# Kernel optimization log

Hardware: AMD Instinct MI355X
Metric: run time of the kernel (lower is better)

The kernel has to match this reference:

```python
import jax, jax.numpy as jnp
import numpy as np

C = 128      # block channels
K = 7        # involution kernel size
GC = 16      # group_ch
G = (C // 2) // GC  # involution groups = 4


def conv1x1(x, w, b):
    # x: (B,Cin,H,W), w: (Cout,Cin)
    return jnp.einsum('bchw,oc->bohw', x, w) + b[None, :, None, None]


def conv2d(x, w, b, pad):
    y = jax.lax.conv_general_dilated(
        x, w, window_strides=(1, 1), padding=((pad, pad), (pad, pad)),
        dimension_numbers=('NCHW', 'OIHW', 'NCHW'))
    return y + b[None, :, None, None]


def prelu(x, a):
    return jnp.where(x >= 0, x, a * x)


def patches7(x):
    # x: (B,C,H,W) -> (B,C,K*K,H,W), same padding (torch Unfold, pad=3)
    B, Cc, H, W = x.shape
    p = K // 2
    xp = jnp.pad(x, ((0, 0), (0, 0), (p, p), (p, p)))
    return jnp.stack([xp[:, :, i:i + H, j:j + W]
                      for i in range(K) for j in range(K)], axis=2)


def setup_inputs() -> dict:
    key = jax.random.key(0)
    ks = jax.random.split(key, 9)
    f32 = jnp.float32
    def w(k, shape, s=0.02):
        return jax.random.normal(k, shape, f32) * s
    d = {}
    d['x'] = jax.random.normal(ks[0], (2, C, 128, 128), f32)
    # conv1: C -> C//2, 1x1
    d['w1'] = w(ks[1], (C // 2, C)); d['b1'] = jnp.zeros((C // 2,), f32)
    d['a1'] = jnp.float32(0.25)  # PReLU (single param)
    # involution reduce: C//2 -> C//4, 1x1 (+ReLU)
    d['wr'] = w(ks[2], (C // 4, C // 2)); d['br'] = jnp.zeros((C // 4,), f32)
    # involution span: C//4 -> G*K*K, 1x1
    d['ws'] = w(ks[3], (G * K * K, C // 4)); d['bs'] = jnp.zeros((G * K * K,), f32)
    d['a2'] = jnp.float32(0.25)
    # conv2: C//2 -> C, 1x1
    d['w2'] = w(ks[4], (C, C // 2)); d['b2'] = jnp.zeros((C,), f32)
    # attn conv: 2 -> 1, 7x7 pad 3
    d['wa'] = w(ks[5], (1, 2, 7, 7)); d['ba'] = jnp.zeros((1,), f32)
    # psec: 3x3 (C//4->C//4) + PReLU + 1x1 (C//4->C)
    d['wp1'] = w(ks[6], (C // 4, C // 4, 3, 3)); d['bp1'] = jnp.zeros((C // 4,), f32)
    d['ap'] = jnp.float32(0.25)
    d['wp2'] = w(ks[7], (C, C // 4)); d['bp2'] = jnp.zeros((C,), f32)
    return d


def reference(x, w1, b1, a1, wr, br, ws, bs, a2, w2, b2, wa, ba, wp1, bp1, ap, wp2, bp2):
    B, _, H, W = x.shape
    x1 = prelu(conv1x1(x, w1, b1), a1)                       # (B, C/2, H, W)
    # involution: per-pixel dynamic kernels
    f = jax.nn.relu(conv1x1(x1, wr, br))                     # (B, C/4, H, W)
    kw = conv1x1(f, ws, bs).reshape(B, G, 1, K * K, H, W)    # dynamic kernels
    pat = patches7(x1).reshape(B, G, GC, K * K, H, W)        # unfolded patches
    x2 = (kw * pat).sum(axis=3).reshape(B, C // 2, H, W)     # multiply-reduce
    x3 = conv1x1(prelu(x2, a2), w2, b2)                      # (B, C, H, W)
    # attention gate on f (ZPool -> 7x7 conv -> sigmoid)
    zp = jnp.concatenate([f.max(axis=1, keepdims=True),
                          f.mean(axis=1, keepdims=True)], axis=1)
    attn = jax.nn.sigmoid(conv2d(zp, wa, ba, 3))             # (B, 1, H, W)
    x4 = x3 * attn
    ps = conv1x1(prelu(conv2d(f, wp1, bp1, 1), ap), wp2, bp2)
    return x4 + ps
```

## Files before the change

kernel.cpp:

```cpp
#include <hip/hip_runtime.h>

#define HW_  16384
#define NPX  32768

__device__ __forceinline__ float prelu_(float x, float a) { return x >= 0.f ? x : a * x; }

__global__ __launch_bounds__(256, 2) void k_conv1(const float* __restrict__ x,
        const float* __restrict__ w1, const float* __restrict__ b1,
        const float* __restrict__ a1p, float* __restrict__ x1) {
    __shared__ float xs[64 * 128];
    __shared__ float wT[128 * 36];
    int split = blockIdx.x >> 8;
    int tile = blockIdx.x & 255;
    int b = tile >> 7;
    int hw0 = (tile & 127) << 7;
    int o0 = split * 32;

    for (int e = threadIdx.x; e < 4096; e += 256) {
        int o = e >> 7, c = e & 127;
        wT[c * 36 + o] = w1[(o0 + o) * 128 + c];
    }
    int pxq = threadIdx.x & 31, outq = threadIdx.x >> 5;
    const float a1 = a1p[0];
    float4 acc[4];
    #pragma unroll
    for (int u = 0; u < 4; ++u) { float bv = b1[o0 + outq * 4 + u]; acc[u] = make_float4(bv, bv, bv, bv); }
    const float4* xb = (const float4*)(x + (b << 21) + hw0);
    #pragma unroll 1
    for (int half = 0; half < 2; ++half) {
        float4 xv[8];
        #pragma unroll
        for (int i = 0; i < 8; ++i) {
            int e = threadIdx.x + i * 256;
            int ch = e >> 5, pq = e & 31;
            xv[i] = xb[((half * 64 + ch) << 12) + pq];
        }
        #pragma unroll
        for (int i = 0; i < 8; ++i) {
            int e = threadIdx.x + i * 256;
            int ch = e >> 5, pq = e & 31;
            *(float4*)&xs[ch * 128 + pq * 4] = xv[i];
        }
        __syncthreads();
        #pragma unroll 8
        for (int c2 = 0; c2 < 64; ++c2) {
            float4 tap = *(const float4*)&xs[c2 * 128 + pxq * 4];
            float4 wv  = *(const float4*)&wT[(half * 64 + c2) * 36 + outq * 4];
            acc[0].x = fmaf(wv.x, tap.x, acc[0].x); acc[0].y = fmaf(wv.x, tap.y, acc[0].y);
            acc[0].z = fmaf(wv.x, tap.z, acc[0].z); acc[0].w = fmaf(wv.x, tap.w, acc[0].w);
            acc[1].x = fmaf(wv.y, tap.x, acc[1].x); acc[1].y = fmaf(wv.y, tap.y, acc[1].y);
            acc[1].z = fmaf(wv.y, tap.z, acc[1].z); acc[1].w = fmaf(wv.y, tap.w, acc[1].w);
            acc[2].x = fmaf(wv.z, tap.x, acc[2].x); acc[2].y = fmaf(wv.z, tap.y, acc[2].y);
            acc[2].z = fmaf(wv.z, tap.z, acc[2].z); acc[2].w = fmaf(wv.z, tap.w, acc[2].w);
            acc[3].x = fmaf(wv.w, tap.x, acc[3].x); acc[3].y = fmaf(wv.w, tap.y, acc[3].y);
            acc[3].z = fmaf(wv.w, tap.z, acc[3].z); acc[3].w = fmaf(wv.w, tap.w, acc[3].w);
        }
        __syncthreads();
    }
    #pragma unroll
    for (int u = 0; u < 4; ++u) {
        float4 r;
        r.x = prelu_(acc[u].x, a1); r.y = prelu_(acc[u].y, a1);
        r.z = prelu_(acc[u].z, a1); r.w = prelu_(acc[u].w, a1);
        *(float4*)(x1 + ((b * 64 + o0 + outq * 4 + u) << 14) + hw0 + pxq * 4) = r;
    }
}

__global__ __launch_bounds__(256, 4) void k_reduce(const float* __restrict__ x1,
        const float* __restrict__ wr, const float* __restrict__ br,
        float* __restrict__ f) {
    int tid = blockIdx.x * 256 + threadIdx.x;
    int p2 = tid & 16383;
    int q = tid >> 14;
    int b = p2 >> 13;
    int hw = (p2 & 8191) << 1;
    int o0 = q * 4;
    float2 acc[4];
    #pragma unroll
    for (int u = 0; u < 4; ++u) { float bv = br[o0 + u]; acc[u] = make_float2(bv, bv); }
    const float2* xp = (const float2*)(x1 + (b << 20) + hw);
    #pragma unroll 1
    for (int cb = 0; cb < 4; ++cb) {
        float2 xv[16];
        #pragma unroll
        for (int j = 0; j < 16; ++j) xv[j] = xp[(cb * 16 + j) << 13];
        #pragma unroll
        for (int j = 0; j < 16; ++j) {
            int c = cb * 16 + j;
            #pragma unroll
            for (int u = 0; u < 4; ++u) {
                float wv = wr[(o0 + u) * 64 + c];
                acc[u].x = fmaf(wv, xv[j].x, acc[u].x);
                acc[u].y = fmaf(wv, xv[j].y, acc[u].y);
            }
        }
    }
    float2* op = (float2*)(f + (b << 19) + hw);
    #pragma unroll
    for (int u = 0; u < 4; ++u) {
        float2 r;
        r.x = fmaxf(acc[u].x, 0.f); r.y = fmaxf(acc[u].y, 0.f);
        op[(o0 + u) << 13] = r;
    }
}

__global__ __launch_bounds__(256) void k_invol(const float* __restrict__ x1,
        const float* __restrict__ f, const float* __restrict__ ws_,
        const float* __restrict__ bs, float* __restrict__ x2,
        float* __restrict__ zp) {
    __shared__ float tile[16 * 22 * 24];
    int g = blockIdx.x >> 7;
    int t = blockIdx.x & 127;
    int b = t >> 6;
    int th = (t >> 3) & 7, tw = t & 7;
    int h0 = th * 16, w0 = tw * 16;
    const float* x1g = x1 + ((b * 64 + g * 16) << 14);
    #pragma unroll 1
    for (int rem = threadIdx.x; rem < 484; rem += 256) {
        int r = rem / 22, cl = rem - r * 22;
        int hh = h0 + r - 3, ww = w0 + cl - 3;
        bool ok = (hh >= 0 && hh < 128 && ww >= 0 && ww < 128);
        const float* src = x1g + (hh << 7) + ww;
        float v[16];
        #pragma unroll
        for (int c = 0; c < 16; ++c) v[c] = ok ? src[c << 14] : 0.f;
        float* dst = tile + r * 24 + cl;
        #pragma unroll
        for (int c = 0; c < 16; ++c) dst[c * 528] = v[c];
    }
    int lh = threadIdx.x >> 4, lw = threadIdx.x & 15;
    int hw = ((h0 + lh) << 7) + w0 + lw;
    float fv[32];
    const float* fp = f + (b << 19) + hw;
    #pragma unroll
    for (int c = 0; c < 32; ++c) fv[c] = fp[c << 14];
    if (g == 0) {
        float mx = fv[0], sm = fv[0];
        #pragma unroll
        for (int c = 1; c < 32; ++c) { mx = fmaxf(mx, fv[c]); sm += fv[c]; }
        zp[((b * 2 + 0) << 14) + hw] = mx;
        zp[((b * 2 + 1) << 14) + hw] = sm * (1.f / 32.f);
    }
    __syncthreads();
    float acc[16];
    #pragma unroll
    for (int u = 0; u < 16; ++u) acc[u] = 0.f;
    const float* tap0 = tile + lh * 24 + lw;
    const float* wk = ws_ + g * 49 * 32;
    const float* bsg = bs + g * 49;
    #pragma unroll 1
    for (int di = 0; di < 7; ++di) {
        #pragma unroll 1
        for (int dj = 0; dj < 7; ++dj) {
            int kk = di * 7 + dj;
            float kwv = bsg[kk];
            const float* wkk = wk + kk * 32;
            #pragma unroll
            for (int c = 0; c < 32; ++c) kwv = fmaf(wkk[c], fv[c], kwv);
            const float* tp = tap0 + di * 24 + dj;
            #pragma unroll
            for (int u = 0; u < 16; ++u)
                acc[u] = fmaf(kwv, tp[u * 528], acc[u]);
        }
    }
    float* op = x2 + ((b * 64 + g * 16) << 14) + hw;
    #pragma unroll
    for (int u = 0; u < 16; ++u) op[u << 14] = acc[u];
}

__global__ __launch_bounds__(256) void k_attn(const float* __restrict__ zp,
        const float* __restrict__ wa, const float* __restrict__ ba,
        float* __restrict__ attn) {
    __shared__ float zs[2][22 * 23];
    int t = blockIdx.x;
    int b = t >> 6;
    int tile = t & 63;
    int th = tile >> 3, tw = tile & 7;
    int h0 = th * 16, w0 = tw * 16;
    const float* zb = zp + (b << 15);
    #pragma unroll 1
    for (int rem = threadIdx.x; rem < 484; rem += 256) {
        int r = rem / 22, cl = rem - r * 22;
        int hh = h0 + r - 3, ww = w0 + cl - 3;
        bool ok = (hh >= 0 && hh < 128 && ww >= 0 && ww < 128);
        const float* src = zb + (hh << 7) + ww;
        float v0 = ok ? src[0] : 0.f;
        float v1 = ok ? src[HW_] : 0.f;
        zs[0][r * 23 + cl] = v0;
        zs[1][r * 23 + cl] = v1;
    }
    __syncthreads();
    int lh = threadIdx.x >> 4, lw = threadIdx.x & 15;
    float acc = ba[0];
    #pragma unroll
    for (int c = 0; c < 2; ++c) {
        const float* zc = &zs[c][lh * 23 + lw];
        #pragma unroll
        for (int i = 0; i < 7; ++i)
            #pragma unroll
            for (int j = 0; j < 7; ++j)
                acc = fmaf(wa[c * 49 + i * 7 + j], zc[i * 23 + j], acc);
    }
    attn[(b << 14) + ((h0 + lh) << 7) + w0 + lw] = 1.f / (1.f + expf(-acc));
}

__global__ __launch_bounds__(256) void k_psec1(const float* __restrict__ f,
        const float* __restrict__ wp1, const float* __restrict__ bp1,
        const float* __restrict__ app, float* __restrict__ p1) {
    __shared__ float fs[32 * 190];
    __shared__ float wT[288 * 16];
    int half = blockIdx.x >> 8;
    int t = blockIdx.x & 255;
    int b = t >> 7;
    int tile = t & 127;
    int th = tile >> 3, tw = tile & 7;
    int h0 = th * 8, w0 = tw * 16;
    int o0 = half * 16;

    const float4* wsrc4 = (const float4*)(wp1 + o0 * 288);
    #pragma unroll 1
    for (int e4 = threadIdx.x; e4 < 1152; e4 += 256) {
        float4 v = wsrc4[e4];
        int o = e4 / 72, r4 = (e4 - o * 72) * 4;
        wT[(r4 + 0) * 16 + o] = v.x;
        wT[(r4 + 1) * 16 + o] = v.y;
        wT[(r4 + 2) * 16 + o] = v.z;
        wT[(r4 + 3) * 16 + o] = v.w;
    }
    const float* fb = f + (b << 19);
    #pragma unroll 1
    for (int rem = threadIdx.x; rem < 180; rem += 256) {
        int r = rem / 18, cl = rem - r * 18;
        int hh = h0 + r - 1, ww = w0 + cl - 1;
        bool ok = (hh >= 0 && hh < 128 && ww >= 0 && ww < 128);
        const float* src = fb + (hh << 7) + ww;
        float* dst = fs + r * 19 + cl;
        #pragma unroll 1
        for (int cb = 0; cb < 4; ++cb) {
            float v[8];
            #pragma unroll
            for (int c = 0; c < 8; ++c) v[c] = ok ? src[(cb * 8 + c) << 14] : 0.f;
            #pragma unroll
            for (int c = 0; c < 8; ++c) dst[(cb * 8 + c) * 190] = v[c];
        }
    }
    __syncthreads();

    int pxq = threadIdx.x & 31;
    int rowq = pxq >> 2, colq = pxq & 3;
    int oh = threadIdx.x >> 5;
    const float ap = app[0];
    float acc[2][4];
    #pragma unroll
    for (int o = 0; o < 2; ++o) {
        float bv = bp1[o0 + oh * 2 + o];
        #pragma unroll
        for (int px = 0; px < 4; ++px) acc[o][px] = bv;
    }
    const float* fsb = fs + rowq * 19 + colq * 4;
    for (int ci = 0; ci < 32; ++ci) {
        float tap[3][6];
        const float* base = fsb + ci * 190;
        #pragma unroll
        for (int r = 0; r < 3; ++r)
            #pragma unroll
            for (int j = 0; j < 6; ++j)
                tap[r][j] = base[r * 19 + j];
        #pragma unroll
        for (int ki = 0; ki < 3; ++ki)
            #pragma unroll
            for (int kj = 0; kj < 3; ++kj) {
                float2 wv = *(const float2*)&wT[((ci * 9 + ki * 3 + kj) << 4) + oh * 2];
                #pragma unroll
                for (int px = 0; px < 4; ++px) {
                    float tv = tap[ki][px + kj];
                    acc[0][px] = fmaf(wv.x, tv, acc[0][px]);
                    acc[1][px] = fmaf(wv.y, tv, acc[1][px]);
                }
            }
    }
    int hw = ((h0 + rowq) << 7) + w0 + colq * 4;
    #pragma unroll
    for (int o = 0; o < 2; ++o) {
        float4 r;
        r.x = prelu_(acc[o][0], ap); r.y = prelu_(acc[o][1], ap);
        r.z = prelu_(acc[o][2], ap); r.w = prelu_(acc[o][3], ap);
        *(float4*)(p1 + ((b * 32 + o0 + oh * 2 + o) << 14) + hw) = r;
    }
}

__global__ __launch_bounds__(256, 2) void k_final(const float* __restrict__ x2,
        const float* __restrict__ p1, const float* __restrict__ attn,
        const float* __restrict__ a2p, const float* __restrict__ w2,
        const float* __restrict__ b2, const float* __restrict__ wp2,
        const float* __restrict__ bp2, float* __restrict__ out) {
    __shared__ float xs2[64 * 128];
    __shared__ float ps[32 * 128];
    __shared__ float wT2[64 * 36];
    __shared__ float wTp[32 * 36];
    __shared__ float as_[128];
    int split = blockIdx.x >> 8;
    int tile = blockIdx.x & 255;
    int b = tile >> 7;
    int hw0 = (tile & 127) << 7;
    int o0 = split * 32;
    const float a2 = a2p[0];

    for (int e = threadIdx.x; e < 2048; e += 256) {
        int o = e >> 6, c = e & 63;
        wT2[c * 36 + o] = w2[(o0 + o) * 64 + c];
    }
    for (int e = threadIdx.x; e < 1024; e += 256) {
        int o = e >> 5, c = e & 31;
        wTp[c * 36 + o] = wp2[(o0 + o) * 32 + c];
    }
    {
        const float4* xb = (const float4*)(x2 + (b << 20) + hw0);
        float4 xv[8];
        #pragma unroll
        for (int i = 0; i < 8; ++i) {
            int e = threadIdx.x + i * 256;
            xv[i] = xb[((e >> 5) << 12) + (e & 31)];
        }
        #pragma unroll
        for (int i = 0; i < 8; ++i) {
            int e = threadIdx.x + i * 256;
            float4 v = xv[i];
            v.x = prelu_(v.x, a2); v.y = prelu_(v.y, a2);
            v.z = prelu_(v.z, a2); v.w = prelu_(v.w, a2);
            *(float4*)&xs2[(e >> 5) * 128 + (e & 31) * 4] = v;
        }
        const float4* pb = (const float4*)(p1 + (b << 19) + hw0);
        float4 pv[4];
        #pragma unroll
        for (int i = 0; i < 4; ++i) {
            int e = threadIdx.x + i * 256;
            pv[i] = pb[((e >> 5) << 12) + (e & 31)];
        }
        #pragma unroll
        for (int i = 0; i < 4; ++i) {
            int e = threadIdx.x + i * 256;
            *(float4*)&ps[(e >> 5) * 128 + (e & 31) * 4] = pv[i];
        }
        if (threadIdx.x < 32)
            ((float4*)as_)[threadIdx.x] = ((const float4*)(attn + (b << 14) + hw0))[threadIdx.x];
    }
    int pxq = threadIdx.x & 31, outq = threadIdx.x >> 5;
    float b2v[4], bpv[4];
    #pragma unroll
    for (int u = 0; u < 4; ++u) { b2v[u] = b2[o0 + outq * 4 + u]; bpv[u] = bp2[o0 + outq * 4 + u]; }
    __syncthreads();

    float4 acc[4];
    #pragma unroll
    for (int u = 0; u < 4; ++u) acc[u] = make_float4(0.f, 0.f, 0.f, 0.f);
    #pragma unroll 8
    for (int c = 0; c < 64; ++c) {
        float4 tap = *(const float4*)&xs2[c * 128 + pxq * 4];
        float4 wv  = *(const float4*)&wT2[c * 36 + outq * 4];
        acc[0].x = fmaf(wv.x, tap.x, acc[0].x); acc[0].y = fmaf(wv.x, tap.y, acc[0].y);
        acc[0].z = fmaf(wv.x, tap.z, acc[0].z); acc[0].w = fmaf(wv.x, tap.w, acc[0].w);
        acc[1].x = fmaf(wv.y, tap.x, acc[1].x); acc[1].y = fmaf(wv.y, tap.y, acc[1].y);
        acc[1].z = fmaf(wv.y, tap.z, acc[1].z); acc[1].w = fmaf(wv.y, tap.w, acc[1].w);
        acc[2].x = fmaf(wv.z, tap.x, acc[2].x); acc[2].y = fmaf(wv.z, tap.y, acc[2].y);
        acc[2].z = fmaf(wv.z, tap.z, acc[2].z); acc[2].w = fmaf(wv.z, tap.w, acc[2].w);
        acc[3].x = fmaf(wv.w, tap.x, acc[3].x); acc[3].y = fmaf(wv.w, tap.y, acc[3].y);
        acc[3].z = fmaf(wv.w, tap.z, acc[3].z); acc[3].w = fmaf(wv.w, tap.w, acc[3].w);
    }
    float4 at = *(const float4*)&as_[pxq * 4];
    #pragma unroll
    for (int u = 0; u < 4; ++u) {
        acc[u].x = (acc[u].x + b2v[u]) * at.x + bpv[u];
        acc[u].y = (acc[u].y + b2v[u]) * at.y + bpv[u];
        acc[u].z = (acc[u].z + b2v[u]) * at.z + bpv[u];
        acc[u].w = (acc[u].w + b2v[u]) * at.w + bpv[u];
    }
    #pragma unroll 8
    for (int c = 0; c < 32; ++c) {
        float4 tap = *(const float4*)&ps[c * 128 + pxq * 4];
        float4 wv  = *(const float4*)&wTp[c * 36 + outq * 4];
        acc[0].x = fmaf(wv.x, tap.x, acc[0].x); acc[0].y = fmaf(wv.x, tap.y, acc[0].y);
        acc[0].z = fmaf(wv.x, tap.z, acc[0].z); acc[0].w = fmaf(wv.x, tap.w, acc[0].w);
        acc[1].x = fmaf(wv.y, tap.x, acc[1].x); acc[1].y = fmaf(wv.y, tap.y, acc[1].y);
        acc[1].z = fmaf(wv.y, tap.z, acc[1].z); acc[1].w = fmaf(wv.y, tap.w, acc[1].w);
        acc[2].x = fmaf(wv.z, tap.x, acc[2].x); acc[2].y = fmaf(wv.z, tap.y, acc[2].y);
        acc[2].z = fmaf(wv.z, tap.z, acc[2].z); acc[2].w = fmaf(wv.z, tap.w, acc[2].w);
        acc[3].x = fmaf(wv.w, tap.x, acc[3].x); acc[3].y = fmaf(wv.w, tap.y, acc[3].y);
        acc[3].z = fmaf(wv.w, tap.z, acc[3].z); acc[3].w = fmaf(wv.w, tap.w, acc[3].w);
    }
    #pragma unroll
    for (int u = 0; u < 4; ++u)
        *(float4*)(out + ((b * 128 + o0 + outq * 4 + u) << 14) + hw0 + pxq * 4) = acc[u];
}

extern "C" void kernel_launch(void* const* d_in, const int* in_sizes, int n_in,
                              void* d_out, int out_size, void* d_ws, size_t ws_size,
                              hipStream_t stream) {
    const float* x   = (const float*)d_in[0];
    const float* w1  = (const float*)d_in[1];
    const float* b1  = (const float*)d_in[2];
    const float* a1  = (const float*)d_in[3];
    const float* wr  = (const float*)d_in[4];
    const float* br  = (const float*)d_in[5];
    const float* ws_ = (const float*)d_in[6];
    const float* bs  = (const float*)d_in[7];
    const float* a2  = (const float*)d_in[8];
    const float* w2  = (const float*)d_in[9];
    const float* b2  = (const float*)d_in[10];
    const float* wa  = (const float*)d_in[11];
    const float* ba  = (const float*)d_in[12];
    const float* wp1 = (const float*)d_in[13];
    const float* bp1 = (const float*)d_in[14];
    const float* ap  = (const float*)d_in[15];
    const float* wp2 = (const float*)d_in[16];
    const float* bp2 = (const float*)d_in[17];
    float* out = (float*)d_out;

    float* w = (float*)d_ws;
    float* ws_x1   = w;
    float* ws_f    = ws_x1 + 2 * 64 * HW_;
    float* ws_x2   = ws_f  + 2 * 32 * HW_;
    float* ws_zp   = ws_x2 + 2 * 64 * HW_;
    float* ws_attn = ws_zp + 2 * 2 * HW_;
    float* ws_p1   = ws_attn + NPX;

    hipLaunchKernelGGL(k_conv1, dim3(512), dim3(256), 0, stream,
                       x, w1, b1, a1, ws_x1);
    hipLaunchKernelGGL(k_reduce, dim3(8 * 16384 / 256), dim3(256), 0, stream,
                       ws_x1, wr, br, ws_f);
    hipLaunchKernelGGL(k_invol, dim3(512), dim3(256), 0, stream,
                       ws_x1, ws_f, ws_, bs, ws_x2, ws_zp);
    hipLaunchKernelGGL(k_attn, dim3(128), dim3(256), 0, stream,
                       ws_zp, wa, ba, ws_attn);
    hipLaunchKernelGGL(k_psec1, dim3(512), dim3(256), 0, stream,
                       ws_f, wp1, bp1, ap, ws_p1);
    hipLaunchKernelGGL(k_final, dim3(1024), dim3(256), 0, stream,
                       ws_x2, ws_p1, ws_attn, a2, w2, b2, wp2, bp2, out);
}
```

Baseline: 194.5 us.

## Merge involution and 3x3 psec conv into one launch, retile pointwise GEMMs

```diff
diff --git a/kernel.cpp b/kernel.cpp
--- a/kernel.cpp
+++ b/kernel.cpp
@@ -20,11 +20,12 @@
         int o = e >> 7, c = e & 127;
         wT[c * 36 + o] = w1[(o0 + o) * 128 + c];
     }
-    int pxq = threadIdx.x & 31, outq = threadIdx.x >> 5;
+    int pr = threadIdx.x & 63;
+    int og = threadIdx.x >> 6;
     const float a1 = a1p[0];
-    float4 acc[4];
-    #pragma unroll
-    for (int u = 0; u < 4; ++u) { float bv = b1[o0 + outq * 4 + u]; acc[u] = make_float4(bv, bv, bv, bv); }
+    float2 acc[8];
+    #pragma unroll
+    for (int u = 0; u < 8; ++u) { float bv = b1[o0 + og * 8 + u]; acc[u] = make_float2(bv, bv); }
     const float4* xb = (const float4*)(x + (b << 21) + hw0);
     #pragma unroll 1
     for (int half = 0; half < 2; ++half) {
@@ -32,37 +33,36 @@
         #pragma unroll
         for (int i = 0; i < 8; ++i) {
             int e = threadIdx.x + i * 256;
-            int ch = e >> 5, pq = e & 31;
-            xv[i] = xb[((half * 64 + ch) << 12) + pq];
-        }
+            xv[i] = xb[((half * 64 + (e >> 5)) << 12) + (e & 31)];
+        }
+        __syncthreads();
         #pragma unroll
         for (int i = 0; i < 8; ++i) {
             int e = threadIdx.x + i * 256;
-            int ch = e >> 5, pq = e & 31;
-            *(float4*)&xs[ch * 128 + pq * 4] = xv[i];
+            *(float4*)&xs[(e >> 5) * 128 + (e & 31) * 4] = xv[i];
         }
         __syncthreads();
         #pragma unroll 8
         for (int c2 = 0; c2 < 64; ++c2) {
-            float4 tap = *(const float4*)&xs[c2 * 128 + pxq * 4];
-            float4 wv  = *(const float4*)&wT[(half * 64 + c2) * 36 + outq * 4];
-            acc[0].x = fmaf(wv.x, tap.x, acc[0].x); acc[0].y = fmaf(wv.x, tap.y, acc[0].y);
-            acc[0].z = fmaf(wv.x, tap.z, acc[0].z); acc[0].w = fmaf(wv.x, tap.w, acc[0].w);
-            acc[1].x = fmaf(wv.y, tap.x, acc[1].x); acc[1].y = fmaf(wv.y, tap.y, acc[1].y);
-            acc[1].z = fmaf(wv.y, tap.z, acc[1].z); acc[1].w = fmaf(wv.y, tap.w, acc[1].w);
-            acc[2].x = fmaf(wv.z, tap.x, acc[2].x); acc[2].y = fmaf(wv.z, tap.y, acc[2].y);
-            acc[2].z = fmaf(wv.z, tap.z, acc[2].z); acc[2].w = fmaf(wv.z, tap.w, acc[2].w);
-            acc[3].x = fmaf(wv.w, tap.x, acc[3].x); acc[3].y = fmaf(wv.w, tap.y, acc[3].y);
-            acc[3].z = fmaf(wv.w, tap.z, acc[3].z); acc[3].w = fmaf(wv.w, tap.w, acc[3].w);
-        }
-        __syncthreads();
-    }
-    #pragma unroll
-    for (int u = 0; u < 4; ++u) {
-        float4 r;
+            float2 tap = *(const float2*)&xs[c2 * 128 + pr * 2];
+            const float* wb = &wT[(half * 64 + c2) * 36 + og * 8];
+            float4 wva = *(const float4*)wb;
+            float4 wvb = *(const float4*)(wb + 4);
+            acc[0].x = fmaf(wva.x, tap.x, acc[0].x); acc[0].y = fmaf(wva.x, tap.y, acc[0].y);
+            acc[1].x = fmaf(wva.y, tap.x, acc[1].x); acc[1].y = fmaf(wva.y, tap.y, acc[1].y);
+            acc[2].x = fmaf(wva.z, tap.x, acc[2].x); acc[2].y = fmaf(wva.z, tap.y, acc[2].y);
+            acc[3].x = fmaf(wva.w, tap.x, acc[3].x); acc[3].y = fmaf(wva.w, tap.y, acc[3].y);
+            acc[4].x = fmaf(wvb.x, tap.x, acc[4].x); acc[4].y = fmaf(wvb.x, tap.y, acc[4].y);
+            acc[5].x = fmaf(wvb.y, tap.x, acc[5].x); acc[5].y = fmaf(wvb.y, tap.y, acc[5].y);
+            acc[6].x = fmaf(wvb.z, tap.x, acc[6].x); acc[6].y = fmaf(wvb.z, tap.y, acc[6].y);
+            acc[7].x = fmaf(wvb.w, tap.x, acc[7].x); acc[7].y = fmaf(wvb.w, tap.y, acc[7].y);
+        }
+    }
+    #pragma unroll
+    for (int u = 0; u < 8; ++u) {
+        float2 r;
         r.x = prelu_(acc[u].x, a1); r.y = prelu_(acc[u].y, a1);
-        r.z = prelu_(acc[u].z, a1); r.w = prelu_(acc[u].w, a1);
-        *(float4*)(x1 + ((b * 64 + o0 + outq * 4 + u) << 14) + hw0 + pxq * 4) = r;
+        *(float2*)(x1 + ((b * 64 + o0 + og * 8 + u) << 14) + hw0 + pr * 2) = r;
     }
 }
 
@@ -104,68 +104,167 @@
     }
 }
 
-__global__ __launch_bounds__(256) void k_invol(const float* __restrict__ x1,
+__global__ __launch_bounds__(256) void k_mid(const float* __restrict__ x1,
         const float* __restrict__ f, const float* __restrict__ ws_,
         const float* __restrict__ bs, float* __restrict__ x2,
-        float* __restrict__ zp) {
-    __shared__ float tile[16 * 22 * 24];
-    int g = blockIdx.x >> 7;
-    int t = blockIdx.x & 127;
-    int b = t >> 6;
-    int th = (t >> 3) & 7, tw = t & 7;
-    int h0 = th * 16, w0 = tw * 16;
-    const float* x1g = x1 + ((b * 64 + g * 16) << 14);
-    #pragma unroll 1
-    for (int rem = threadIdx.x; rem < 484; rem += 256) {
-        int r = rem / 22, cl = rem - r * 22;
-        int hh = h0 + r - 3, ww = w0 + cl - 3;
-        bool ok = (hh >= 0 && hh < 128 && ww >= 0 && ww < 128);
-        const float* src = x1g + (hh << 7) + ww;
-        float v[16];
-        #pragma unroll
-        for (int c = 0; c < 16; ++c) v[c] = ok ? src[c << 14] : 0.f;
-        float* dst = tile + r * 24 + cl;
-        #pragma unroll
-        for (int c = 0; c < 16; ++c) dst[c * 528] = v[c];
-    }
-    int lh = threadIdx.x >> 4, lw = threadIdx.x & 15;
-    int hw = ((h0 + lh) << 7) + w0 + lw;
-    float fv[32];
-    const float* fp = f + (b << 19) + hw;
-    #pragma unroll
-    for (int c = 0; c < 32; ++c) fv[c] = fp[c << 14];
-    if (g == 0) {
-        float mx = fv[0], sm = fv[0];
-        #pragma unroll
-        for (int c = 1; c < 32; ++c) { mx = fmaxf(mx, fv[c]); sm += fv[c]; }
-        zp[((b * 2 + 0) << 14) + hw] = mx;
-        zp[((b * 2 + 1) << 14) + hw] = sm * (1.f / 32.f);
-    }
-    __syncthreads();
-    float acc[16];
-    #pragma unroll
-    for (int u = 0; u < 16; ++u) acc[u] = 0.f;
-    const float* tap0 = tile + lh * 24 + lw;
-    const float* wk = ws_ + g * 49 * 32;
-    const float* bsg = bs + g * 49;
-    #pragma unroll 1
-    for (int di = 0; di < 7; ++di) {
+        float* __restrict__ zp, const float* __restrict__ wp1,
+        const float* __restrict__ bp1, const float* __restrict__ app,
+        float* __restrict__ p1) {
+    __shared__ float smem[14432];
+    if (blockIdx.x < 256) {
+        float* tile = smem;
+        int g = blockIdx.x >> 6;
+        int t = blockIdx.x & 63;
+        int b = t >> 5;
+        int tl = t & 31;
+        int th = tl >> 2, tw = tl & 3;
+        int h0 = th * 16, w0 = tw * 32;
+        const float* x1g = x1 + ((b * 64 + g * 16) << 14);
         #pragma unroll 1
-        for (int dj = 0; dj < 7; ++dj) {
-            int kk = di * 7 + dj;
-            float kwv = bsg[kk];
-            const float* wkk = wk + kk * 32;
-            #pragma unroll
-            for (int c = 0; c < 32; ++c) kwv = fmaf(wkk[c], fv[c], kwv);
-            const float* tp = tap0 + di * 24 + dj;
-            #pragma unroll
-            for (int u = 0; u < 16; ++u)
-                acc[u] = fmaf(kwv, tp[u * 528], acc[u]);
-        }
-    }
-    float* op = x2 + ((b * 64 + g * 16) << 14) + hw;
-    #pragma unroll
-    for (int u = 0; u < 16; ++u) op[u << 14] = acc[u];
+        for (int rem = threadIdx.x; rem < 836; rem += 256) {
+            int r = rem / 38, cl = rem - r * 38;
+            int hh = h0 + r - 3, ww = w0 + cl - 3;
+            bool ok = (hh >= 0 && hh < 128 && ww >= 0 && ww < 128);
+            const float* src = x1g + (hh << 7) + ww;
+            float v[16];
+            #pragma unroll
+            for (int c = 0; c < 16; ++c) v[c] = ok ? src[c << 14] : 0.f;
+            float* dst = tile + r * 41 + cl;
+            #pragma unroll
+            for (int c = 0; c < 16; ++c) dst[c * 902] = v[c];
+        }
+        int lh = threadIdx.x >> 4;
+        int pc = threadIdx.x & 15;
+        int hw = ((h0 + lh) << 7) + w0 + pc * 2;
+        float2 fv[32];
+        const float* fp = f + (b << 19) + hw;
+        #pragma unroll
+        for (int c = 0; c < 32; ++c) fv[c] = *(const float2*)&fp[c << 14];
+        if (g == 0) {
+            float2 mx = fv[0], sm = fv[0];
+            #pragma unroll
+            for (int c = 1; c < 32; ++c) {
+                mx.x = fmaxf(mx.x, fv[c].x); mx.y = fmaxf(mx.y, fv[c].y);
+                sm.x += fv[c].x; sm.y += fv[c].y;
+            }
+            *(float2*)&zp[((b * 2 + 0) << 14) + hw] = mx;
+            sm.x *= (1.f / 32.f); sm.y *= (1.f / 32.f);
+            *(float2*)&zp[((b * 2 + 1) << 14) + hw] = sm;
+        }
+        __syncthreads();
+        float2 acc[16];
+        #pragma unroll
+        for (int u = 0; u < 16; ++u) acc[u] = make_float2(0.f, 0.f);
+        const float* tap0 = tile + lh * 41 + pc * 2;
+        const float* wk = ws_ + g * 49 * 32;
+        const float* bsg = bs + g * 49;
+        #pragma unroll 1
+        for (int di = 0; di < 7; ++di) {
+            #pragma unroll 1
+            for (int dj = 0; dj < 7; ++dj) {
+                int kk = di * 7 + dj;
+                float bsv = bsg[kk];
+                float2 kwv = make_float2(bsv, bsv);
+                const float* wkk = wk + kk * 32;
+                #pragma unroll
+                for (int c = 0; c < 32; ++c) {
+                    float wc = wkk[c];
+                    kwv.x = fmaf(wc, fv[c].x, kwv.x);
+                    kwv.y = fmaf(wc, fv[c].y, kwv.y);
+                }
+                const float* tp = tap0 + di * 41 + dj;
+                #pragma unroll
+                for (int u = 0; u < 16; ++u) {
+                    float t0 = tp[u * 902], t1 = tp[u * 902 + 1];
+                    acc[u].x = fmaf(kwv.x, t0, acc[u].x);
+                    acc[u].y = fmaf(kwv.y, t1, acc[u].y);
+                }
+            }
+        }
+        float* op = x2 + ((b * 64 + g * 16) << 14) + hw;
+        #pragma unroll
+        for (int u = 0; u < 16; ++u) *(float2*)&op[u << 14] = acc[u];
+    } else {
+        float* fs = smem;
+        float* wT = smem + 6080;
+        int bid = blockIdx.x - 256;
+        int half = bid >> 8;
+        int t = bid & 255;
+        int b = t >> 7;
+        int tl = t & 127;
+        int th = tl >> 3, tw = tl & 7;
+        int h0 = th * 8, w0 = tw * 16;
+        int o0 = half * 16;
+        const float4* wsrc4 = (const float4*)(wp1 + o0 * 288);
+        #pragma unroll 1
+        for (int e4 = threadIdx.x; e4 < 1152; e4 += 256) {
+            float4 v = wsrc4[e4];
+            int o = e4 / 72, r4 = (e4 - o * 72) * 4;
+            wT[(r4 + 0) * 16 + o] = v.x;
+            wT[(r4 + 1) * 16 + o] = v.y;
+            wT[(r4 + 2) * 16 + o] = v.z;
+            wT[(r4 + 3) * 16 + o] = v.w;
+        }
+        const float* fb = f + (b << 19);
+        #pragma unroll 1
+        for (int rem = threadIdx.x; rem < 180; rem += 256) {
+            int r = rem / 18, cl = rem - r * 18;
+            int hh = h0 + r - 1, ww = w0 + cl - 1;
+            bool ok = (hh >= 0 && hh < 128 && ww >= 0 && ww < 128);
+            const float* src = fb + (hh << 7) + ww;
+            float* dst = fs + r * 19 + cl;
+            #pragma unroll 1
+            for (int cb = 0; cb < 4; ++cb) {
+                float v[8];
+                #pragma unroll
+                for (int c = 0; c < 8; ++c) v[c] = ok ? src[(cb * 8 + c) << 14] : 0.f;
+                #pragma unroll
+                for (int c = 0; c < 8; ++c) dst[(cb * 8 + c) * 190] = v[c];
+            }
+        }
+        __syncthreads();
+        int pxq = threadIdx.x & 31;
+        int rowq = pxq >> 2, colq = pxq & 3;
+        int oh = threadIdx.x >> 5;
+        const float ap = app[0];
+        float acc[2][4];
+        #pragma unroll
+        for (int o = 0; o < 2; ++o) {
+            float bv = bp1[o0 + oh * 2 + o];
+            #pragma unroll
+            for (int px = 0; px < 4; ++px) acc[o][px] = bv;
+        }
+        const float* fsb = fs + rowq * 19 + colq * 4;
+        for (int ci = 0; ci < 32; ++ci) {
+            float tap[3][6];
+            const float* base = fsb + ci * 190;
+            #pragma unroll
+            for (int r = 0; r < 3; ++r)
+                #pragma unroll
+                for (int j = 0; j < 6; ++j)
+                    tap[r][j] = base[r * 19 + j];
+            #pragma unroll
+            for (int ki = 0; ki < 3; ++ki)
+                #pragma unroll
+                for (int kj = 0; kj < 3; ++kj) {
+                    float2 wv = *(const float2*)&wT[((ci * 9 + ki * 3 + kj) << 4) + oh * 2];
+                    #pragma unroll
+                    for (int px = 0; px < 4; ++px) {
+                        float tv = tap[ki][px + kj];
+                        acc[0][px] = fmaf(wv.x, tv, acc[0][px]);
+                        acc[1][px] = fmaf(wv.y, tv, acc[1][px]);
+                    }
+                }
+        }
+        int hw = ((h0 + rowq) << 7) + w0 + colq * 4;
+        #pragma unroll
+        for (int o = 0; o < 2; ++o) {
+            float4 r;
+            r.x = prelu_(acc[o][0], ap); r.y = prelu_(acc[o][1], ap);
+            r.z = prelu_(acc[o][2], ap); r.w = prelu_(acc[o][3], ap);
+            *(float4*)(p1 + ((b * 32 + o0 + oh * 2 + o) << 14) + hw) = r;
+        }
+    }
 }
 
 __global__ __launch_bounds__(256) void k_attn(const float* __restrict__ zp,
@@ -204,91 +303,6 @@
     attn[(b << 14) + ((h0 + lh) << 7) + w0 + lw] = 1.f / (1.f + expf(-acc));
 }
 
-__global__ __launch_bounds__(256) void k_psec1(const float* __restrict__ f,
-        const float* __restrict__ wp1, const float* __restrict__ bp1,
-        const float* __restrict__ app, float* __restrict__ p1) {
-    __shared__ float fs[32 * 190];
-    __shared__ float wT[288 * 16];
-    int half = blockIdx.x >> 8;
-    int t = blockIdx.x & 255;
-    int b = t >> 7;
-    int tile = t & 127;
-    int th = tile >> 3, tw = tile & 7;
-    int h0 = th * 8, w0 = tw * 16;
-    int o0 = half * 16;
-
-    const float4* wsrc4 = (const float4*)(wp1 + o0 * 288);
-    #pragma unroll 1
-    for (int e4 = threadIdx.x; e4 < 1152; e4 += 256) {
-        float4 v = wsrc4[e4];
-        int o = e4 / 72, r4 = (e4 - o * 72) * 4;
-        wT[(r4 + 0) * 16 + o] = v.x;
-        wT[(r4 + 1) * 16 + o] = v.y;
-        wT[(r4 + 2) * 16 + o] = v.z;
-        wT[(r4 + 3) * 16 + o] = v.w;
-    }
-    const float* fb = f + (b << 19);
-    #pragma unroll 1
-    for (int rem = threadIdx.x; rem < 180; rem += 256) {
-        int r = rem / 18, cl = rem - r * 18;
-        int hh = h0 + r - 1, ww = w0 + cl - 1;
-        bool ok = (hh >= 0 && hh < 128 && ww >= 0 && ww < 128);
-        const float* src = fb + (hh << 7) + ww;
-        float* dst = fs + r * 19 + cl;
-        #pragma unroll 1
-        for (int cb = 0; cb < 4; ++cb) {
-            float v[8];
-            #pragma unroll
-            for (int c = 0; c < 8; ++c) v[c] = ok ? src[(cb * 8 + c) << 14] : 0.f;
-            #pragma unroll
-            for (int c = 0; c < 8; ++c) dst[(cb * 8 + c) * 190] = v[c];
-        }
-    }
-    __syncthreads();
-
-    int pxq = threadIdx.x & 31;
-    int rowq = pxq >> 2, colq = pxq & 3;
-    int oh = threadIdx.x >> 5;
-    const float ap = app[0];
-    float acc[2][4];
-    #pragma unroll
-    for (int o = 0; o < 2; ++o) {
-        float bv = bp1[o0 + oh * 2 + o];
-        #pragma unroll
-        for (int px = 0; px < 4; ++px) acc[o][px] = bv;
-    }
-    const float* fsb = fs + rowq * 19 + colq * 4;
-    for (int ci = 0; ci < 32; ++ci) {
-        float tap[3][6];
-        const float* base = fsb + ci * 190;
-        #pragma unroll
-        for (int r = 0; r < 3; ++r)
-            #pragma unroll
-            for (int j = 0; j < 6; ++j)
-                tap[r][j] = base[r * 19 + j];
-        #pragma unroll
-        for (int ki = 0; ki < 3; ++ki)
-            #pragma unroll
-            for (int kj = 0; kj < 3; ++kj) {
-                float2 wv = *(const float2*)&wT[((ci * 9 + ki * 3 + kj) << 4) + oh * 2];
-                #pragma unroll
-                for (int px = 0; px < 4; ++px) {
-                    float tv = tap[ki][px + kj];
-                    acc[0][px] = fmaf(wv.x, tv, acc[0][px]);
-                    acc[1][px] = fmaf(wv.y, tv, acc[1][px]);
-                }
-            }
-    }
-    int hw = ((h0 + rowq) << 7) + w0 + colq * 4;
-    #pragma unroll
-    for (int o = 0; o < 2; ++o) {
-        float4 r;
-        r.x = prelu_(acc[o][0], ap); r.y = prelu_(acc[o][1], ap);
-        r.z = prelu_(acc[o][2], ap); r.w = prelu_(acc[o][3], ap);
-        *(float4*)(p1 + ((b * 32 + o0 + oh * 2 + o) << 14) + hw) = r;
-    }
-}
-
 __global__ __launch_bounds__(256, 2) void k_final(const float* __restrict__ x2,
         const float* __restrict__ p1, const float* __restrict__ attn,
         const float* __restrict__ a2p, const float* __restrict__ w2,
@@ -345,52 +359,55 @@
         if (threadIdx.x < 32)
             ((float4*)as_)[threadIdx.x] = ((const float4*)(attn + (b << 14) + hw0))[threadIdx.x];
     }
-    int pxq = threadIdx.x & 31, outq = threadIdx.x >> 5;
-    float b2v[4], bpv[4];
-    #pragma unroll
-    for (int u = 0; u < 4; ++u) { b2v[u] = b2[o0 + outq * 4 + u]; bpv[u] = bp2[o0 + outq * 4 + u]; }
+    int pr = threadIdx.x & 63;
+    int og = threadIdx.x >> 6;
+    float b2v[8], bpv[8];
+    #pragma unroll
+    for (int u = 0; u < 8; ++u) { b2v[u] = b2[o0 + og * 8 + u]; bpv[u] = bp2[o0 + og * 8 + u]; }
     __syncthreads();
 
-    float4 acc[4];
-    #pragma unroll
-    for (int u = 0; u < 4; ++u) acc[u] = make_float4(0.f, 0.f, 0.f, 0.f);
+    float2 acc[8];
+    #pragma unroll
+    for (int u = 0; u < 8; ++u) acc[u] = make_float2(0.f, 0.f);
     #pragma unroll 8
     for (int c = 0; c < 64; ++c) {
-        float4 tap = *(const float4*)&xs2[c * 128 + pxq * 4];
-        float4 wv  = *(const float4*)&wT2[c * 36 + outq * 4];
-        acc[0].x = fmaf(wv.x, tap.x, acc[0].x); acc[0].y = fmaf(wv.x, tap.y, acc[0].y);
-        acc[0].z = fmaf(wv.x, tap.z, acc[0].z); acc[0].w = fmaf(wv.x, tap.w, acc[0].w);
-        acc[1].x = fmaf(wv.y, tap.x, acc[1].x); acc[1].y = fmaf(wv.y, tap.y, acc[1].y);
-        acc[1].z = fmaf(wv.y, tap.z, acc[1].z); acc[1].w = fmaf(wv.y, tap.w, acc[1].w);
-        acc[2].x = fmaf(wv.z, tap.x, acc[2].x); acc[2].y = fmaf(wv.z, tap.y, acc[2].y);
-        acc[2].z = fmaf(wv.z, tap.z, acc[2].z); acc[2].w = fmaf(wv.z, tap.w, acc[2].w);
-        acc[3].x = fmaf(wv.w, tap.x, acc[3].x); acc[3].y = fmaf(wv.w, tap.y, acc[3].y);
-        acc[3].z = fmaf(wv.w, tap.z, acc[3].z); acc[3].w = fmaf(wv.w, tap.w, acc[3].w);
-    }
-    float4 at = *(const float4*)&as_[pxq * 4];
-    #pragma unroll
-    for (int u = 0; u < 4; ++u) {
+        float2 tap = *(const float2*)&xs2[c * 128 + pr * 2];
+        const float* wb = &wT2[c * 36 + og * 8];
+        float4 wva = *(const float4*)wb;
+        float4 wvb = *(const float4*)(wb + 4);
+        acc[0].x = fmaf(wva.x, tap.x, acc[0].x); acc[0].y = fmaf(wva.x, tap.y, acc[0].y);
+        acc[1].x = fmaf(wva.y, tap.x, acc[1].x); acc[1].y = fmaf(wva.y, tap.y, acc[1].y);
+        acc[2].x = fmaf(wva.z, tap.x, acc[2].x); acc[2].y = fmaf(wva.z, tap.y, acc[2].y);
+        acc[3].x = fmaf(wva.w, tap.x, acc[3].x); acc[3].y = fmaf(wva.w, tap.y, acc[3].y);
+        acc[4].x = fmaf(wvb.x, tap.x, acc[4].x); acc[4].y = fmaf(wvb.x, tap.y, acc[4].y);
+        acc[5].x = fmaf(wvb.y, tap.x, acc[5].x); acc[5].y = fmaf(wvb.y, tap.y, acc[5].y);
+        acc[6].x = fmaf(wvb.z, tap.x, acc[6].x); acc[6].y = fmaf(wvb.z, tap.y, acc[6].y);
+        acc[7].x = fmaf(wvb.w, tap.x, acc[7].x); acc[7].y = fmaf(wvb.w, tap.y, acc[7].y);
+    }
+    float2 at = *(const float2*)&as_[pr * 2];
+    #pragma unroll
+    for (int u = 0; u < 8; ++u) {
         acc[u].x = (acc[u].x + b2v[u]) * at.x + bpv[u];
         acc[u].y = (acc[u].y + b2v[u]) * at.y + bpv[u];
-        acc[u].z = (acc[u].z + b2v[u]) * at.z + bpv[u];
-        acc[u].w = (acc[u].w + b2v[u]) * at.w + bpv[u];
     }
     #pragma unroll 8
     for (int c = 0; c < 32; ++c) {
-        float4 tap = *(const float4*)&ps[c * 128 + pxq * 4];
-        float4 wv  = *(const float4*)&wTp[c * 36 + outq * 4];
-        acc[0].x = fmaf(wv.x, tap.x, acc[0].x); acc[0].y = fmaf(wv.x, tap.y, acc[0].y);
-        acc[0].z = fmaf(wv.x, tap.z, acc[0].z); acc[0].w = fmaf(wv.x, tap.w, acc[0].w);
-        acc[1].x = fmaf(wv.y, tap.x, acc[1].x); acc[1].y = fmaf(wv.y, tap.y, acc[1].y);
-        acc[1].z = fmaf(wv.y, tap.z, acc[1].z); acc[1].w = fmaf(wv.y, tap.w, acc[1].w);
-        acc[2].x = fmaf(wv.z, tap.x, acc[2].x); acc[2].y = fmaf(wv.z, tap.y, acc[2].y);
-        acc[2].z = fmaf(wv.z, tap.z, acc[2].z); acc[2].w = fmaf(wv.z, tap.w, acc[2].w);
-        acc[3].x = fmaf(wv.w, tap.x, acc[3].x); acc[3].y = fmaf(wv.w, tap.y, acc[3].y);
-        acc[3].z = fmaf(wv.w, tap.z, acc[3].z); acc[3].w = fmaf(wv.w, tap.w, acc[3].w);
-    }
-    #pragma unroll
-    for (int u = 0; u < 4; ++u)
-        *(float4*)(out + ((b * 128 + o0 + outq * 4 + u) << 14) + hw0 + pxq * 4) = acc[u];
+        float2 tap = *(const float2*)&ps[c * 128 + pr * 2];
+        const float* wb = &wTp[c * 36 + og * 8];
+        float4 wva = *(const float4*)wb;
+        float4 wvb = *(const float4*)(wb + 4);
+        acc[0].x = fmaf(wva.x, tap.x, acc[0].x); acc[0].y = fmaf(wva.x, tap.y, acc[0].y);
+        acc[1].x = fmaf(wva.y, tap.x, acc[1].x); acc[1].y = fmaf(wva.y, tap.y, acc[1].y);
+        acc[2].x = fmaf(wva.z, tap.x, acc[2].x); acc[2].y = fmaf(wva.z, tap.y, acc[2].y);
+        acc[3].x = fmaf(wva.w, tap.x, acc[3].x); acc[3].y = fmaf(wva.w, tap.y, acc[3].y);
+        acc[4].x = fmaf(wvb.x, tap.x, acc[4].x); acc[4].y = fmaf(wvb.x, tap.y, acc[4].y);
+        acc[5].x = fmaf(wvb.y, tap.x, acc[5].x); acc[5].y = fmaf(wvb.y, tap.y, acc[5].y);
+        acc[6].x = fmaf(wvb.z, tap.x, acc[6].x); acc[6].y = fmaf(wvb.z, tap.y, acc[6].y);
+        acc[7].x = fmaf(wvb.w, tap.x, acc[7].x); acc[7].y = fmaf(wvb.w, tap.y, acc[7].y);
+    }
+    #pragma unroll
+    for (int u = 0; u < 8; ++u)
+        *(float2*)(out + ((b * 128 + o0 + og * 8 + u) << 14) + hw0 + pr * 2) = acc[u];
 }
 
 extern "C" void kernel_launch(void* const* d_in, const int* in_sizes, int n_in,
@@ -428,12 +445,11 @@
                        x, w1, b1, a1, ws_x1);
     hipLaunchKernelGGL(k_reduce, dim3(8 * 16384 / 256), dim3(256), 0, stream,
                        ws_x1, wr, br, ws_f);
-    hipLaunchKernelGGL(k_invol, dim3(512), dim3(256), 0, stream,
-                       ws_x1, ws_f, ws_, bs, ws_x2, ws_zp);
+    hipLaunchKernelGGL(k_mid, dim3(768), dim3(256), 0, stream,
+                       ws_x1, ws_f, ws_, bs, ws_x2, ws_zp,
+                       wp1, bp1, ap, ws_p1);
     hipLaunchKernelGGL(k_attn, dim3(128), dim3(256), 0, stream,
                        ws_zp, wa, ba, ws_attn);
-    hipLaunchKernelGGL(k_psec1, dim3(512), dim3(256), 0, stream,
-                       ws_f, wp1, bp1, ap, ws_p1);
     hipLaunchKernelGGL(k_final, dim3(1024), dim3(256), 0, stream,
                        ws_x2, ws_p1, ws_attn, a2, w2, b2, wp2, bp2, out);
 }
```

After: 196.8 us. About the same (+1.2%).
